# Optimization experiments

Measured on AMD Instinct MI355X. Metric: run time of the kernel, lower is better.

## Reference

```python
import jax, jax.numpy as jnp
import numpy as np

S = 7
BATCH = 8192
LAMBDA_COORD = 5.0
LAMBDA_NOOBJ = 0.5
EPS = 1e-06


def setup_inputs() -> dict:
    key = jax.random.key(0)
    k1, k2, k3 = jax.random.split(key, 3)
    predicts = jax.random.uniform(k1, (BATCH, S, S, 30), dtype=jnp.float32)
    targets = jax.random.uniform(k2, (BATCH, S, S, 30), dtype=jnp.float32)
    keep = jax.random.uniform(k3, (BATCH, S, S)) < 0.25
    conf = jnp.where(keep, targets[..., 4], 0.0)
    targets = targets.at[..., 4].set(conf).at[..., 9].set(conf)
    return {"predicts": predicts, "targets": targets}


def _cxcywh_to_xyxy(cx, cy, w, h):
    return cx - w / 2, cy - h / 2, cx + w / 2, cy + h / 2


def _elementwise_iou(a, b):
    # a, b: tuples (cx, cy, w, h) of [batch, S, S] arrays.
    # Equivalent to torchvision box_iou(A, B).diag() but computed per-cell (no N^2 matrix).
    ax1, ay1, ax2, ay2 = _cxcywh_to_xyxy(*a)
    bx1, by1, bx2, by2 = _cxcywh_to_xyxy(*b)
    iw = jnp.clip(jnp.minimum(ax2, bx2) - jnp.maximum(ax1, bx1), 0.0)
    ih = jnp.clip(jnp.minimum(ay2, by2) - jnp.maximum(ay1, by1), 0.0)
    inter = iw * ih
    area_a = (ax2 - ax1) * (ay2 - ay1)
    area_b = (bx2 - bx1) * (by2 - by1)
    return inter / (area_a + area_b - inter)


def reference(predicts, targets):
    pre1 = predicts[..., :5]
    pre2 = predicts[..., 5:10]
    pre_cls = predicts[..., 10:]
    tar = targets[..., :5]
    tar_cls = targets[..., 10:]

    obj = targets[..., 4] > 0  # [B, S, S]
    noobj = ~obj

    gx = jnp.arange(S, dtype=predicts.dtype)[None, :]  # grid_x, broadcast over rows
    gy = jnp.arange(S, dtype=predicts.dtype)[:, None]  # grid_y, broadcast over cols
    ratio = 1.0 / S

    def to_abs(b):
        return ((b[..., 0] + gx) * ratio, (b[..., 1] + gy) * ratio, b[..., 2], b[..., 3])

    abs1, abs2, abst = to_abs(pre1), to_abs(pre2), to_abs(tar)
    iou1 = _elementwise_iou(abs1, abst)  # [B, S, S]
    iou2 = _elementwise_iou(abs2, abst)
    resp = iou1 > iou2

    m1 = (obj & resp).astype(predicts.dtype)   # box1 responsible
    m2 = (obj & ~resp).astype(predicts.dtype)  # box2 responsible
    mo = obj.astype(predicts.dtype)
    mn = noobj.astype(predicts.dtype)

    # coordinate losses (sum-reduced masked MSE)
    loss_xy = jnp.sum(m1[..., None] * (pre1[..., :2] - tar[..., :2]) ** 2) + \
              jnp.sum(m2[..., None] * (pre2[..., :2] - tar[..., :2]) ** 2)
    sq = lambda x: jnp.sqrt(jnp.clip(x, EPS))
    loss_wh = jnp.sum(m1[..., None] * (sq(pre1[..., 2:4]) - sq(tar[..., 2:4])) ** 2) + \
              jnp.sum(m2[..., None] * (sq(pre2[..., 2:4]) - sq(tar[..., 2:4])) ** 2)
    coord_loss = LAMBDA_COORD * (loss_xy + loss_wh)

    # confidence losses (note: IoU target is NOT detached in the original)
    conf_obj = jnp.sum(m1 * (pre1[..., 4] - iou1) ** 2) + \
               jnp.sum(m2 * (pre2[..., 4] - iou2) ** 2)
    conf_noobj = LAMBDA_NOOBJ * (jnp.sum(mn * pre1[..., 4] ** 2) +
                                 jnp.sum(mn * pre2[..., 4] ** 2))

    # class loss
    cls_loss = jnp.sum(mo[..., None] * (pre_cls - tar_cls) ** 2)

    return coord_loss + conf_obj + conf_noobj + cls_loss
```

## Files before the change

### kernel.cpp

```cpp
#include <hip/hip_runtime.h>
#include <math.h>


#define S7 7
#define CCH 30
#define CELLS_PER_BLOCK 256
#define N_CELLS (8192 * S7 * S7)
#define N_BLOCKS (N_CELLS / CELLS_PER_BLOCK)
#define EPSV 1e-6f

__device__ __forceinline__ float iou_cxcywh(float acx, float acy, float aw, float ah,
                                            float bcx, float bcy, float bw, float bh) {
    float ax1 = acx - aw * 0.5f, ax2 = acx + aw * 0.5f;
    float ay1 = acy - ah * 0.5f, ay2 = acy + ah * 0.5f;
    float bx1 = bcx - bw * 0.5f, bx2 = bcx + bw * 0.5f;
    float by1 = bcy - bh * 0.5f, by2 = bcy + bh * 0.5f;
    float iw = fmaxf(fminf(ax2, bx2) - fmaxf(ax1, bx1), 0.0f);
    float ih = fmaxf(fminf(ay2, by2) - fmaxf(ay1, by1), 0.0f);
    float inter = iw * ih;
    float area_a = (ax2 - ax1) * (ay2 - ay1);
    float area_b = (bx2 - bx1) * (by2 - by1);
    return inter / (area_a + area_b - inter);
}

__global__ __launch_bounds__(256) void yolo_loss_partial(const float* __restrict__ pred,
                                                         const float* __restrict__ targ,
                                                         float* __restrict__ partial) {
    __shared__ float smem[2 * CELLS_PER_BLOCK * CCH];

    const int tid = threadIdx.x;
    const int lane = tid & 63;
    const int wid = tid >> 6;
    const int block_cell0 = blockIdx.x * CELLS_PER_BLOCK;

    const float* gp = pred + (size_t)block_cell0 * CCH;
    const float* gt = targ + (size_t)block_cell0 * CCH;

#pragma unroll
    for (int i = 0; i < 15; ++i) {
        const int c = wid * 15 + i;
        const float* gsrc = (c < 30) ? (gp + c * 256 + lane * 4)
                                     : (gt + (c - 30) * 256 + lane * 4);
        float* ldst = smem + c * 256;
        __builtin_amdgcn_global_load_lds(
            (const __attribute__((address_space(1))) void*)gsrc,
            (__attribute__((address_space(3))) void*)ldst,
            16, 0, 0);
    }
    __syncthreads();

    const float* p = smem + tid * CCH;
    const float* t = smem + CELLS_PER_BLOCK * CCH + tid * CCH;
    const int cell = block_cell0 + tid;
    const int xy = cell % (S7 * S7);
    const float fx = (float)(xy % S7);
    const float fy = (float)(xy / S7);
    const float ratio = 1.0f / 7.0f;

    float px1 = p[0], py1 = p[1], pw1 = p[2], ph1 = p[3], pc1 = p[4];
    float px2 = p[5], py2 = p[6], pw2 = p[7], ph2 = p[8], pc2 = p[9];
    float tx = t[0], ty = t[1], tw = t[2], th = t[3], tc = t[4];
    bool obj = tc > 0.0f;

    float tcx = (tx + fx) * ratio, tcy = (ty + fy) * ratio;
    float iou1 = iou_cxcywh((px1 + fx) * ratio, (py1 + fy) * ratio, pw1, ph1,
                            tcx, tcy, tw, th);
    float iou2 = iou_cxcywh((px2 + fx) * ratio, (py2 + fy) * ratio, pw2, ph2,
                            tcx, tcy, tw, th);
    bool resp = iou1 > iou2;

    float cls = 0.0f;
#pragma unroll
    for (int k = 10; k < 30; ++k) {
        float d = p[k] - t[k];
        cls += d * d;
    }

    float loss;
    if (obj) {
        float sx, sy, sw, sh, sc, siou;
        if (resp) { sx = px1; sy = py1; sw = pw1; sh = ph1; sc = pc1; siou = iou1; }
        else      { sx = px2; sy = py2; sw = pw2; sh = ph2; sc = pc2; siou = iou2; }
        float dx = sx - tx, dy = sy - ty;
        float dw = sqrtf(fmaxf(sw, EPSV)) - sqrtf(fmaxf(tw, EPSV));
        float dh = sqrtf(fmaxf(sh, EPSV)) - sqrtf(fmaxf(th, EPSV));
        float dc = sc - siou;
        loss = 5.0f * (dx * dx + dy * dy + dw * dw + dh * dh) + dc * dc + cls;
    } else {
        loss = 0.5f * (pc1 * pc1 + pc2 * pc2);
    }

    float v = loss;
#pragma unroll
    for (int off = 32; off > 0; off >>= 1) v += __shfl_down(v, off);

    __shared__ float red[4];
    if (lane == 0) red[wid] = v;
    __syncthreads();
    if (tid == 0) partial[blockIdx.x] = red[0] + red[1] + red[2] + red[3];
}

__global__ __launch_bounds__(256) void yolo_loss_final(const float* __restrict__ partial,
                                                       float* __restrict__ out) {
    float v = 0.0f;
    for (int i = threadIdx.x; i < N_BLOCKS; i += 256) v += partial[i];
#pragma unroll
    for (int off = 32; off > 0; off >>= 1) v += __shfl_down(v, off);

    __shared__ float red[4];
    const int lane = threadIdx.x & 63;
    const int wid = threadIdx.x >> 6;
    if (lane == 0) red[wid] = v;
    __syncthreads();
    if (threadIdx.x == 0) out[0] = red[0] + red[1] + red[2] + red[3];
}

extern "C" void kernel_launch(void* const* d_in, const int* in_sizes, int n_in,
                              void* d_out, int out_size, void* d_ws, size_t ws_size,
                              hipStream_t stream) {
    const float* predicts = (const float*)d_in[0];
    const float* targets  = (const float*)d_in[1];
    float* out = (float*)d_out;
    float* partial = (float*)d_ws;

    yolo_loss_partial<<<N_BLOCKS, 256, 0, stream>>>(predicts, targets, partial);
    yolo_loss_final<<<1, 256, 0, stream>>>(partial, out);
}
```

Measured before the change: 110.3 us.

## Fuse final reduction via last-block ticket and halve block size

Merges the partial and final reduction kernels into one launch: each block writes its partial sum and takes an atomic ticket, and the last block to finish sums all partials. Block size drops from 256 to 128 cells/threads, so each wave now loads a whole tensor (pred or targ) for its block, and there are twice as many blocks. A memset is added to reset the ticket each call. This removes the second kernel launch and its tail, but adds an atomic per block, a memset node, and a serial final pass over twice as many partials in one block.

Result: slower. 232.0 us (+110.2%).

```diff
diff --git a/kernel.cpp b/kernel.cpp
--- a/kernel.cpp
+++ b/kernel.cpp
@@ -4,7 +4,8 @@
 
 #define S7 7
 #define CCH 30
-#define CELLS_PER_BLOCK 256
+#define CELLS_PER_BLOCK 128
+#define THREADS 128
 #define N_CELLS (8192 * S7 * S7)
 #define N_BLOCKS (N_CELLS / CELLS_PER_BLOCK)
 #define EPSV 1e-6f
@@ -23,29 +24,33 @@
     return inter / (area_a + area_b - inter);
 }
 
-__global__ __launch_bounds__(256) void yolo_loss_partial(const float* __restrict__ pred,
-                                                         const float* __restrict__ targ,
-                                                         float* __restrict__ partial) {
+__global__ __launch_bounds__(THREADS) void yolo_loss_fused(const float* __restrict__ pred,
+                                                           const float* __restrict__ targ,
+                                                           float* __restrict__ partial,
+                                                           unsigned int* __restrict__ ticket,
+                                                           float* __restrict__ out) {
     __shared__ float smem[2 * CELLS_PER_BLOCK * CCH];
+    __shared__ float red[2];
+    __shared__ int is_last;
 
     const int tid = threadIdx.x;
     const int lane = tid & 63;
     const int wid = tid >> 6;
     const int block_cell0 = blockIdx.x * CELLS_PER_BLOCK;
 
-    const float* gp = pred + (size_t)block_cell0 * CCH;
-    const float* gt = targ + (size_t)block_cell0 * CCH;
-
+    {
+        const float* gbase = (wid == 0) ? (pred + (size_t)block_cell0 * CCH)
+                                        : (targ + (size_t)block_cell0 * CCH);
+        float* lbase = smem + wid * (CELLS_PER_BLOCK * CCH);
 #pragma unroll
-    for (int i = 0; i < 15; ++i) {
-        const int c = wid * 15 + i;
-        const float* gsrc = (c < 30) ? (gp + c * 256 + lane * 4)
-                                     : (gt + (c - 30) * 256 + lane * 4);
-        float* ldst = smem + c * 256;
-        __builtin_amdgcn_global_load_lds(
-            (const __attribute__((address_space(1))) void*)gsrc,
-            (__attribute__((address_space(3))) void*)ldst,
-            16, 0, 0);
+        for (int i = 0; i < 15; ++i) {
+            const float* gsrc = gbase + i * 256 + lane * 4;
+            float* ldst = lbase + i * 256;
+            __builtin_amdgcn_global_load_lds(
+                (const __attribute__((address_space(1))) void*)gsrc,
+                (__attribute__((address_space(3))) void*)ldst,
+                16, 0, 0);
+        }
     }
     __syncthreads();
 
@@ -94,25 +99,27 @@
 #pragma unroll
     for (int off = 32; off > 0; off >>= 1) v += __shfl_down(v, off);
 
-    __shared__ float red[4];
     if (lane == 0) red[wid] = v;
     __syncthreads();
-    if (tid == 0) partial[blockIdx.x] = red[0] + red[1] + red[2] + red[3];
-}
 
-__global__ __launch_bounds__(256) void yolo_loss_final(const float* __restrict__ partial,
-                                                       float* __restrict__ out) {
-    float v = 0.0f;
-    for (int i = threadIdx.x; i < N_BLOCKS; i += 256) v += partial[i];
+    if (tid == 0) {
+        partial[blockIdx.x] = red[0] + red[1];
+        __threadfence();
+        unsigned int old = atomicAdd(ticket, 1u);
+        is_last = (old == (unsigned int)(N_BLOCKS - 1));
+    }
+    __syncthreads();
+
+    if (is_last) {
+        __threadfence();
+        float s = 0.0f;
+        for (int i = tid; i < N_BLOCKS; i += THREADS) s += partial[i];
 #pragma unroll
-    for (int off = 32; off > 0; off >>= 1) v += __shfl_down(v, off);
-
-    __shared__ float red[4];
-    const int lane = threadIdx.x & 63;
-    const int wid = threadIdx.x >> 6;
-    if (lane == 0) red[wid] = v;
-    __syncthreads();
-    if (threadIdx.x == 0) out[0] = red[0] + red[1] + red[2] + red[3];
+        for (int off = 32; off > 0; off >>= 1) s += __shfl_down(s, off);
+        if (lane == 0) red[wid] = s;
+        __syncthreads();
+        if (tid == 0) out[0] = red[0] + red[1];
+    }
 }
 
 extern "C" void kernel_launch(void* const* d_in, const int* in_sizes, int n_in,
@@ -122,7 +129,8 @@
     const float* targets  = (const float*)d_in[1];
     float* out = (float*)d_out;
     float* partial = (float*)d_ws;
+    unsigned int* ticket = (unsigned int*)((char*)d_ws + (size_t)N_BLOCKS * 4);
 
-    yolo_loss_partial<<<N_BLOCKS, 256, 0, stream>>>(predicts, targets, partial);
-    yolo_loss_final<<<1, 256, 0, stream>>>(partial, out);
+    hipMemsetAsync(ticket, 0, 4, stream);
+    yolo_loss_fused<<<N_BLOCKS, THREADS, 0, stream>>>(predicts, targets, partial, ticket, out);
 }
```
